# Optimization experiments

Measured on AMD Instinct MI355X. Metric: run time of the kernel, lower is better.

Reference implementation:

```python
import jax, jax.numpy as jnp
import numpy as np

S, R, CM, CZ, C, H = 128, 256, 256, 128, 32, 8
EPS = 1e-5


def layer_norm(x, w, b):
    mu = jnp.mean(x, axis=-1, keepdims=True)
    var = jnp.mean(jnp.square(x - mu), axis=-1, keepdims=True)
    return (x - mu) * jax.lax.rsqrt(var + EPS) * w + b


def setup_inputs() -> dict:
    key = jax.random.key(0)
    ks = jax.random.split(key, 10)
    s = 0.02
    return {
        "m": jax.random.normal(ks[0], (S, R, CM), jnp.float32),
        "z": jax.random.normal(ks[1], (R, R, CZ), jnp.float32),
        "ln_m_w": jnp.ones((CM,), jnp.float32),
        "ln_m_b": jnp.zeros((CM,), jnp.float32),
        "ln_z_w": jnp.ones((CZ,), jnp.float32),
        "ln_z_b": jnp.zeros((CZ,), jnp.float32),
        "Wz": jax.random.normal(ks[2], (CZ, H), jnp.float32) * s,
        "Wq": jax.random.normal(ks[3], (CM, H * C), jnp.float32) * s,
        "Wk": jax.random.normal(ks[4], (CM, H * C), jnp.float32) * s,
        "Wv": jax.random.normal(ks[5], (CM, H * C), jnp.float32) * s,
        "Wg": jax.random.normal(ks[6], (CM, H * C), jnp.float32) * s,
        "bg": jnp.ones((H * C,), jnp.float32),
        "Wo": jax.random.normal(ks[7], (H * C, CM), jnp.float32) * s,
        "bo": jnp.zeros((CM,), jnp.float32),
    }


def reference(m, z, ln_m_w, ln_m_b, ln_z_w, ln_z_b, Wz, Wq, Wk, Wv, Wg, bg, Wo, bo):
    mn = layer_norm(m, ln_m_w, ln_m_b)              # [S,R,CM]
    zn = layer_norm(z, ln_z_w, ln_z_b)              # [R,R,CZ]
    bias = jnp.einsum('qkz,zh->hqk', zn, Wz)        # [H,R,R] pair bias
    q = (mn @ Wq).reshape(S, R, H, C) * (C ** -0.5)
    k = (mn @ Wk).reshape(S, R, H, C)
    v = (mn @ Wv).reshape(S, R, H, C)
    logits = jnp.einsum('sqhc,skhc->shqk', q, k) + bias[None]  # [S,H,R,R]
    a = jax.nn.softmax(logits, axis=-1)
    o = jnp.einsum('shqk,skhc->sqhc', a, v)         # [S,R,H,C]
    g = jax.nn.sigmoid(mn @ Wg + bg).reshape(S, R, H, C)
    return (g * o).reshape(S, R, H * C) @ Wo + bo   # [S,R,CM]
```

## Files before the change

kernel.cpp:

```cpp
#include <hip/hip_runtime.h>
#include <math.h>

#define S_DIM 128
#define R_DIM 256
#define CM_DIM 256
#define CZ_DIM 128
#define C_DIM 32
#define H_DIM 8
#define HC_DIM 256
#define LN_EPS 1e-5f
#define ZPAD 132
#define HSZ 1048576
#define BIAS_SCALE 16384.0f
#define BIAS_INV (1.0f / 16384.0f)

typedef _Float16 half8 __attribute__((ext_vector_type(8)));
typedef _Float16 half4 __attribute__((ext_vector_type(4)));
typedef float f32x4 __attribute__((ext_vector_type(4)));
typedef short short4v __attribute__((ext_vector_type(4)));
typedef short short8v __attribute__((ext_vector_type(8)));

__device__ __forceinline__ float wave_sum(float v) {
#pragma unroll
    for (int off = 32; off > 0; off >>= 1) v += __shfl_down(v, off);
    return v;
}

__global__ __launch_bounds__(256) void convert_w_kernel(const float* __restrict__ Wq,
                                                        const float* __restrict__ Wk,
                                                        const float* __restrict__ Wv,
                                                        const float* __restrict__ Wg,
                                                        const float* __restrict__ Wo,
                                                        _Float16* __restrict__ w3) {
    int kb = blockIdx.x;
    int mat = blockIdx.y;
    const float* src = (mat == 0) ? Wq : (mat == 1) ? Wk : (mat == 2) ? Wv : (mat == 3) ? Wg : Wo;
    int n = threadIdx.x;
    _Float16 tmp[32];
#pragma unroll
    for (int kk = 0; kk < 32; kk++)
        tmp[kk] = (_Float16)src[(size_t)(kb * 32 + kk) * 256 + n];
    half8* dst = (half8*)(w3 + (size_t)mat * 65536 + (size_t)kb * 8192 + (size_t)n * 32);
#pragma unroll
    for (int i = 0; i < 4; i++) dst[i] = *(half8*)&tmp[i * 8];
}

__global__ __launch_bounds__(64) void prep_wz_kernel(const float* __restrict__ w,
                                                     const float* __restrict__ b,
                                                     const float* __restrict__ Wz,
                                                     float* __restrict__ u_g,
                                                     float* __restrict__ UB) {
    int lane = threadIdx.x;
    float w0 = w[lane], w1 = w[lane + 64];
    float b0 = b[lane], b1 = b[lane + 64];
#pragma unroll
    for (int h = 0; h < H_DIM; h++) {
        float wz0 = Wz[lane * H_DIM + h], wz1 = Wz[(lane + 64) * H_DIM + h];
        float u0 = w0 * wz0, u1 = w1 * wz1;
        u_g[h * ZPAD + lane] = u0;
        u_g[h * ZPAD + lane + 64] = u1;
        float U = wave_sum(u0 + u1);
        float B = wave_sum(b0 * wz0 + b1 * wz1);
        if (lane == 0) { UB[h] = U; UB[8 + h] = B; }
    }
}

__global__ __launch_bounds__(64) void ln_m_kernel(const float* __restrict__ m,
                                                  const float* __restrict__ w,
                                                  const float* __restrict__ b,
                                                  _Float16* __restrict__ mn) {
    int row = blockIdx.x;
    int t = threadIdx.x;
    const float4* mrow = (const float4*)(m + (size_t)row * CM_DIM);
    float4 x = mrow[t];
    float s = x.x + x.y + x.z + x.w;
    float ss = x.x * x.x + x.y * x.y + x.z * x.z + x.w * x.w;
    s = wave_sum(s);
    ss = wave_sum(ss);
    s = __shfl(s, 0);
    ss = __shfl(ss, 0);
    float mean = s * (1.0f / CM_DIM);
    float var = ss * (1.0f / CM_DIM) - mean * mean;
    float rsig = rsqrtf(var + LN_EPS);
    float4 wv = ((const float4*)w)[t];
    float4 bv = ((const float4*)b)[t];
    half4 o;
    o[0] = (_Float16)((x.x - mean) * rsig * wv.x + bv.x);
    o[1] = (_Float16)((x.y - mean) * rsig * wv.y + bv.y);
    o[2] = (_Float16)((x.z - mean) * rsig * wv.z + bv.z);
    o[3] = (_Float16)((x.w - mean) * rsig * wv.w + bv.w);
    *(half4*)(mn + (size_t)row * CM_DIM + t * 4) = o;
}

__global__ __launch_bounds__(256) void ln_z_bias_kernel(const float* __restrict__ z,
                                                        const float* __restrict__ u_g,
                                                        const float* __restrict__ UB,
                                                        short* __restrict__ bias_i) {
    __shared__ __align__(16) float zt[64 * ZPAD];
    __shared__ __align__(16) float ut[8 * ZPAD];
    __shared__ float UBs[16];
    int tid = threadIdx.x;
    int row0 = blockIdx.x * 64;
    for (int i = tid; i < 8 * ZPAD; i += 256) ut[i] = u_g[i];
    if (tid < 16) UBs[tid] = UB[tid];
    const float4* zsrc = (const float4*)(z + (size_t)row0 * CZ_DIM);
#pragma unroll
    for (int i = 0; i < 8; i++) {
        int idx = tid + i * 256;
        float4 v = zsrc[idx];
        int r = idx >> 5, c4 = (idx & 31) * 4;
        *(float4*)&zt[r * ZPAD + c4] = v;
    }
    __syncthreads();
    int r = tid >> 2, p = tid & 3;
    const float* zr = &zt[r * ZPAD];
    const float* u0p = &ut[p * ZPAD];
    const float* u1p = &ut[(p + 4) * ZPAD];
    float s = 0.f, ss = 0.f, a0 = 0.f, a1 = 0.f;
#pragma unroll
    for (int c = 0; c < CZ_DIM; c += 4) {
        float4 x = *(const float4*)&zr[c];
        float4 uu0 = *(const float4*)&u0p[c];
        float4 uu1 = *(const float4*)&u1p[c];
        s += x.x + x.y + x.z + x.w;
        ss += x.x * x.x + x.y * x.y + x.z * x.z + x.w * x.w;
        a0 += x.x * uu0.x + x.y * uu0.y + x.z * uu0.z + x.w * uu0.w;
        a1 += x.x * uu1.x + x.y * uu1.y + x.z * uu1.z + x.w * uu1.w;
    }
    float mu = s * (1.0f / CZ_DIM);
    float var = ss * (1.0f / CZ_DIM) - mu * mu;
    float rsig = rsqrtf(var + LN_EPS);
    int row = row0 + r;
    float b0v = rsig * (a0 - mu * UBs[p]) + UBs[8 + p];
    float b1v = rsig * (a1 - mu * UBs[4 + p]) + UBs[12 + p];
    int i0 = (int)rintf(b0v * BIAS_SCALE);
    int i1 = (int)rintf(b1v * BIAS_SCALE);
    i0 = i0 > 32767 ? 32767 : (i0 < -32768 ? -32768 : i0);
    i1 = i1 > 32767 ? 32767 : (i1 < -32768 ? -32768 : i1);
    bias_i[(size_t)p * 65536 + row] = (short)i0;
    bias_i[(size_t)(p + 4) * 65536 + row] = (short)i1;
}

__global__ __launch_bounds__(256, 3) void proj_mfma_kernel(const _Float16* __restrict__ A,
                                                           const _Float16* __restrict__ w3,
                                                           const float* __restrict__ bg,
                                                           _Float16* __restrict__ qh,
                                                           _Float16* __restrict__ kh,
                                                           _Float16* __restrict__ vh,
                                                           _Float16* __restrict__ gh) {
    __shared__ _Float16 As[64][40];
    __shared__ _Float16 Bs[256][40];
    int mat = blockIdx.y;
    int m0 = blockIdx.x * 64;
    const _Float16* W = w3 + (size_t)mat * 65536;
    _Float16* Out = (mat == 0) ? qh : (mat == 1) ? kh : (mat == 2) ? vh : gh;
    int tid = threadIdx.x;
    int lane = tid & 63, wave = tid >> 6;
    int lrow = lane & 15, lk8 = (lane >> 4) * 8;
    f32x4 acc[4][4];
#pragma unroll
    for (int i = 0; i < 4; i++)
#pragma unroll
        for (int j = 0; j < 4; j++) acc[i][j] = (f32x4){0.f, 0.f, 0.f, 0.f};

    for (int kb = 0; kb < 8; kb++) {
        half8 av = *(const half8*)(A + (size_t)(m0 + (tid >> 2)) * 256 + kb * 32 + (tid & 3) * 8);
        half8 bv[4];
#pragma unroll
        for (int i = 0; i < 4; i++)
            bv[i] = *(const half8*)(W + (size_t)kb * 8192 + (size_t)(i * 256 + tid) * 8);
        __syncthreads();
        *(half8*)&As[tid >> 2][(tid & 3) * 8] = av;
#pragma unroll
        for (int i = 0; i < 4; i++) {
            int c = i * 256 + tid;
            *(half8*)&Bs[c >> 2][(c & 3) * 8] = bv[i];
        }
        __syncthreads();
        half8 af[4], bf[4];
#pragma unroll
        for (int mf = 0; mf < 4; mf++) af[mf] = *(half8*)&As[mf * 16 + lrow][lk8];
#pragma unroll
        for (int nf = 0; nf < 4; nf++) bf[nf] = *(half8*)&Bs[wave * 64 + nf * 16 + lrow][lk8];
#pragma unroll
        for (int mf = 0; mf < 4; mf++)
#pragma unroll
            for (int nf = 0; nf < 4; nf++)
                acc[mf][nf] = __builtin_amdgcn_mfma_f32_16x16x32_f16(af[mf], bf[nf], acc[mf][nf], 0, 0, 0);
    }
    const float qscale = 0.17677669529663687f;
#pragma unroll
    for (int mf = 0; mf < 4; mf++)
#pragma unroll
        for (int nf = 0; nf < 4; nf++)
#pragma unroll
            for (int ri = 0; ri < 4; ri++) {
                int row = m0 + mf * 16 + (lane >> 4) * 4 + ri;
                int col = wave * 64 + nf * 16 + lrow;
                float v = acc[mf][nf][ri];
                if (mat == 0) v *= qscale;
                if (mat == 3) {
                    v = 1.0f / (1.0f + __expf(-(v + bg[col])));
                    Out[(size_t)row * 256 + col] = (_Float16)v;
                } else {
                    Out[(size_t)(col >> 5) * HSZ + (size_t)row * 32 + (col & 31)] = (_Float16)v;
                }
            }
}

__global__ __launch_bounds__(512, 1) void attn_mfma_kernel(const _Float16* __restrict__ qh,
                                                           const _Float16* __restrict__ kh,
                                                           const _Float16* __restrict__ vh,
                                                           const short* __restrict__ bias_i,
                                                           _Float16* __restrict__ oh) {
    __shared__ short bias_s[256][264];
    __shared__ _Float16 K_s[64][40];
    __shared__ _Float16 VT_s[32][72];
    int h = blockIdx.x, sg = blockIdx.y;
    int tid = threadIdx.x;
    int lane = tid & 63, wave = tid >> 6;
    int lrow = lane & 15, g = lane >> 4, lk8 = g * 8;
    int qw = wave * 32;

    const short* bsrc = bias_i + (size_t)h * 65536;
#pragma unroll
    for (int i = 0; i < 16; i++) {
        int e = (tid + i * 512) * 8;
        short8v v = *(const short8v*)(bsrc + e);
        *(short8v*)&bias_s[e >> 8][e & 255] = v;
    }

    const _Float16* qbase = qh + (size_t)h * HSZ;
    const _Float16* kbase = kh + (size_t)h * HSZ;
    const _Float16* vbase = vh + (size_t)h * HSZ;
    _Float16* obase = oh + (size_t)h * HSZ;

    bool isK = (wave < 4);
    int key = (tid & 255) >> 2, koff = (tid & 3) * 8;
    int vkey = tid & 63, vc0 = ((tid >> 6) & 3) * 8;

    for (int si = 0; si < 4; si++) {
        int s = sg * 4 + si;
        half8 qfr[2];
#pragma unroll
        for (int qf = 0; qf < 2; qf++)
            qfr[qf] = *(const half8*)(qbase + (size_t)(s * 256 + qw + qf * 16 + lrow) * 32 + lk8);

        f32x4 oaccT[2][2];
        float m_run[2], l_run[2];
#pragma unroll
        for (int qf = 0; qf < 2; qf++) {
            oaccT[qf][0] = (f32x4){0.f, 0.f, 0.f, 0.f};
            oaccT[qf][1] = (f32x4){0.f, 0.f, 0.f, 0.f};
            m_run[qf] = -1e30f;
            l_run[qf] = 0.f;
        }

        half8 stg;
        if (isK) stg = *(const half8*)(kbase + (size_t)(s * 256 + key) * 32 + koff);
        else     stg = *(const half8*)(vbase + (size_t)(s * 256 + vkey) * 32 + vc0);

        for (int kb = 0; kb < 4; kb++) {
            __syncthreads();
            if (isK) {
                *(half8*)&K_s[key][koff] = stg;
            } else {
#pragma unroll
                for (int j = 0; j < 8; j++) VT_s[vc0 + j][vkey] = stg[j];
            }
            if (kb < 3) {
                int nk = (kb + 1) * 64;
                if (isK) stg = *(const half8*)(kbase + (size_t)(s * 256 + nk + key) * 32 + koff);
                else     stg = *(const half8*)(vbase + (size_t)(s * 256 + nk + vkey) * 32 + vc0);
            }
            __syncthreads();

            half8 kfr[4];
#pragma unroll
            for (int kf = 0; kf < 4; kf++) kfr[kf] = *(half8*)&K_s[kf * 16 + lrow][lk8];

#pragma unroll
            for (int qf = 0; qf < 2; qf++) {
                f32x4 sf[4];
#pragma unroll
                for (int kf = 0; kf < 4; kf++) {
                    f32x4 zero = (f32x4){0.f, 0.f, 0.f, 0.f};
                    sf[kf] = __builtin_amdgcn_mfma_f32_16x16x32_f16(kfr[kf], qfr[qf], zero, 0, 0, 0);
                }
                int q = qw + qf * 16 + lrow;
#pragma unroll
                for (int kf = 0; kf < 4; kf++) {
                    short4v bh = *(short4v*)&bias_s[q][kb * 64 + kf * 16 + 4 * g];
#pragma unroll
                    for (int ri = 0; ri < 4; ri++) sf[kf][ri] += (float)bh[ri] * BIAS_INV;
                }
                float tm = -1e30f;
#pragma unroll
                for (int kf = 0; kf < 4; kf++)
#pragma unroll
                    for (int ri = 0; ri < 4; ri++) tm = fmaxf(tm, sf[kf][ri]);
                tm = fmaxf(tm, __shfl_xor(tm, 16));
                tm = fmaxf(tm, __shfl_xor(tm, 32));
                float nm = fmaxf(m_run[qf], tm);
                float sc = __expf(m_run[qf] - nm);
                m_run[qf] = nm;
                oaccT[qf][0] *= sc;
                oaccT[qf][1] *= sc;
                float p[4][4];
                float rs = 0.f;
#pragma unroll
                for (int kf = 0; kf < 4; kf++)
#pragma unroll
                    for (int ri = 0; ri < 4; ri++) {
                        float pv = __expf(sf[kf][ri] - nm);
                        p[kf][ri] = pv;
                        rs += pv;
                    }
                rs += __shfl_xor(rs, 16);
                rs += __shfl_xor(rs, 32);
                l_run[qf] = l_run[qf] * sc + rs;
                unsigned w8[8];
#pragma unroll
                for (int kf = 0; kf < 4; kf++)
#pragma unroll
                    for (int t = 0; t < 2; t++) {
                        union { _Float16 hh[2]; unsigned u; } pk;
                        pk.hh[0] = (_Float16)p[kf][2 * t];
                        pk.hh[1] = (_Float16)p[kf][2 * t + 1];
                        w8[2 * kf + t] = pk.u;
                    }
#pragma unroll
                for (int ks = 0; ks < 2; ks++) {
                    union { unsigned u[4]; half8 h8; } pb;
#pragma unroll
                    for (int u = 0; u < 4; u++) {
                        int srcl = ((g & 1) * 2 + (u >> 1)) * 16 + lrow;
                        unsigned lo_sh = (unsigned)__shfl((int)w8[4 * ks + (u & 1)], srcl);
                        unsigned hi_sh = (unsigned)__shfl((int)w8[4 * ks + (u & 1) + 2], srcl);
                        pb.u[u] = (g >> 1) ? hi_sh : lo_sh;
                    }
#pragma unroll
                    for (int cf = 0; cf < 2; cf++) {
                        half8 va = *(half8*)&VT_s[cf * 16 + lrow][ks * 32 + lk8];
                        oaccT[qf][cf] =
                            __builtin_amdgcn_mfma_f32_16x16x32_f16(va, pb.h8, oaccT[qf][cf], 0, 0, 0);
                    }
                }
            }
        }
#pragma unroll
        for (int qf = 0; qf < 2; qf++) {
            float inv = 1.0f / l_run[qf];
            int q = qw + qf * 16 + lrow;
#pragma unroll
            for (int cf = 0; cf < 2; cf++) {
                half4 o4;
#pragma unroll
                for (int ri = 0; ri < 4; ri++) o4[ri] = (_Float16)(oaccT[qf][cf][ri] * inv);
                *(half4*)(obase + (size_t)(s * 256 + q) * 32 + cf * 16 + 4 * g) = o4;
            }
        }
    }
}

__global__ __launch_bounds__(256, 3) void out_mfma_kernel(const _Float16* __restrict__ gh,
                                                          const _Float16* __restrict__ oh,
                                                          const _Float16* __restrict__ w3o,
                                                          const float* __restrict__ bo,
                                                          float* __restrict__ out) {
    __shared__ _Float16 As[64][40];
    __shared__ _Float16 Bs[256][40];
    int m0 = blockIdx.x * 64;
    int tid = threadIdx.x;
    int lane = tid & 63, wave = tid >> 6;
    int lrow = lane & 15, lk8 = (lane >> 4) * 8;
    f32x4 acc[4][4];
#pragma unroll
    for (int i = 0; i < 4; i++)
#pragma unroll
        for (int j = 0; j < 4; j++) acc[i][j] = (f32x4){0.f, 0.f, 0.f, 0.f};

    for (int kb = 0; kb < 8; kb++) {
        int arow = m0 + (tid >> 2);
        half8 gv = *(const half8*)(gh + (size_t)arow * 256 + kb * 32 + (tid & 3) * 8);
        half8 ov = *(const half8*)(oh + (size_t)kb * HSZ + (size_t)arow * 32 + (tid & 3) * 8);
        half8 av = gv * ov;
        half8 bv[4];
#pragma unroll
        for (int i = 0; i < 4; i++)
            bv[i] = *(const half8*)(w3o + (size_t)kb * 8192 + (size_t)(i * 256 + tid) * 8);
        __syncthreads();
        *(half8*)&As[tid >> 2][(tid & 3) * 8] = av;
#pragma unroll
        for (int i = 0; i < 4; i++) {
            int c = i * 256 + tid;
            *(half8*)&Bs[c >> 2][(c & 3) * 8] = bv[i];
        }
        __syncthreads();
        half8 af[4], bf[4];
#pragma unroll
        for (int mf = 0; mf < 4; mf++) af[mf] = *(half8*)&As[mf * 16 + lrow][lk8];
#pragma unroll
        for (int nf = 0; nf < 4; nf++) bf[nf] = *(half8*)&Bs[wave * 64 + nf * 16 + lrow][lk8];
#pragma unroll
        for (int mf = 0; mf < 4; mf++)
#pragma unroll
            for (int nf = 0; nf < 4; nf++)
                acc[mf][nf] = __builtin_amdgcn_mfma_f32_16x16x32_f16(af[mf], bf[nf], acc[mf][nf], 0, 0, 0);
    }
#pragma unroll
    for (int mf = 0; mf < 4; mf++)
#pragma unroll
        for (int nf = 0; nf < 4; nf++)
#pragma unroll
            for (int ri = 0; ri < 4; ri++) {
                int row = m0 + mf * 16 + (lane >> 4) * 4 + ri;
                int col = wave * 64 + nf * 16 + lrow;
                out[(size_t)row * 256 + col] = acc[mf][nf][ri] + bo[col];
            }
}

extern "C" void kernel_launch(void* const* d_in, const int* in_sizes, int n_in,
                              void* d_out, int out_size, void* d_ws, size_t ws_size,
                              hipStream_t stream) {
    const float* m = (const float*)d_in[0];
    const float* z = (const float*)d_in[1];
    const float* ln_m_w = (const float*)d_in[2];
    const float* ln_m_b = (const float*)d_in[3];
    const float* ln_z_w = (const float*)d_in[4];
    const float* ln_z_b = (const float*)d_in[5];
    const float* Wz = (const float*)d_in[6];
    const float* Wq = (const float*)d_in[7];
    const float* Wk = (const float*)d_in[8];
    const float* Wv = (const float*)d_in[9];
    const float* Wg = (const float*)d_in[10];
    const float* bg = (const float*)d_in[11];
    const float* Wo = (const float*)d_in[12];
    const float* bo = (const float*)d_in[13];
    float* out = (float*)d_out;

    const size_t NE = (size_t)S_DIM * R_DIM * CM_DIM;
    _Float16* hb = (_Float16*)d_ws;
    _Float16* mn_h = hb;
    _Float16* qh = hb + NE;
    _Float16* kh = hb + 2 * NE;
    _Float16* vh = hb + 3 * NE;
    _Float16* gh = hb + 4 * NE;
    _Float16* oh = hb + 5 * NE;
    _Float16* w3 = hb + 6 * NE;
    float* u_g = (float*)(hb + 6 * NE + 5 * 65536);
    float* UB = u_g + 8 * ZPAD;
    short* bias_i = (short*)(UB + 16);

    hipLaunchKernelGGL(convert_w_kernel, dim3(8, 5), dim3(256), 0, stream,
                       Wq, Wk, Wv, Wg, Wo, w3);
    hipLaunchKernelGGL(prep_wz_kernel, dim3(1), dim3(64), 0, stream,
                       ln_z_w, ln_z_b, Wz, u_g, UB);
    hipLaunchKernelGGL(ln_m_kernel, dim3(S_DIM * R_DIM), dim3(64), 0, stream,
                       m, ln_m_w, ln_m_b, mn_h);
    hipLaunchKernelGGL(ln_z_bias_kernel, dim3(1024), dim3(256), 0, stream,
                       z, u_g, UB, bias_i);
    hipLaunchKernelGGL(proj_mfma_kernel, dim3(512, 4), dim3(256), 0, stream,
                       mn_h, w3, bg, qh, kh, vh, gh);
    hipLaunchKernelGGL(attn_mfma_kernel, dim3(H_DIM, 32), dim3(512), 0, stream,
                       qh, kh, vh, bias_i, oh);
    hipLaunchKernelGGL(out_mfma_kernel, dim3(512), dim3(256), 0, stream,
                       gh, oh, w3 + 4 * 65536, bo, out);
}
```

Baseline: 132.6 us.

## Load MFMA fragments directly from global memory, dropping LDS staging in projection GEMMs

The projection and output GEMM kernels no longer stage A and B tiles through shared memory with two barriers per k-step. Each wave now loads its MFMA fragments straight from global memory, and the k-loop is fully unrolled so the loads can be issued early. This removes the LDS round-trip and the block synchronisation. In exchange, all four waves reload the same A fragments, which raises global/L2 traffic, and the launch_bounds occupancy hint is dropped.

```diff
diff --git a/kernel.cpp b/kernel.cpp
--- a/kernel.cpp
+++ b/kernel.cpp
@@ -141,15 +141,13 @@
     bias_i[(size_t)(p + 4) * 65536 + row] = (short)i1;
 }
 
-__global__ __launch_bounds__(256, 3) void proj_mfma_kernel(const _Float16* __restrict__ A,
-                                                           const _Float16* __restrict__ w3,
-                                                           const float* __restrict__ bg,
-                                                           _Float16* __restrict__ qh,
-                                                           _Float16* __restrict__ kh,
-                                                           _Float16* __restrict__ vh,
-                                                           _Float16* __restrict__ gh) {
-    __shared__ _Float16 As[64][40];
-    __shared__ _Float16 Bs[256][40];
+__global__ __launch_bounds__(256) void proj_mfma_kernel(const _Float16* __restrict__ A,
+                                                        const _Float16* __restrict__ w3,
+                                                        const float* __restrict__ bg,
+                                                        _Float16* __restrict__ qh,
+                                                        _Float16* __restrict__ kh,
+                                                        _Float16* __restrict__ vh,
+                                                        _Float16* __restrict__ gh) {
     int mat = blockIdx.y;
     int m0 = blockIdx.x * 64;
     const _Float16* W = w3 + (size_t)mat * 65536;
@@ -163,25 +161,16 @@
 #pragma unroll
         for (int j = 0; j < 4; j++) acc[i][j] = (f32x4){0.f, 0.f, 0.f, 0.f};
 
+#pragma unroll
     for (int kb = 0; kb < 8; kb++) {
-        half8 av = *(const half8*)(A + (size_t)(m0 + (tid >> 2)) * 256 + kb * 32 + (tid & 3) * 8);
-        half8 bv[4];
-#pragma unroll
-        for (int i = 0; i < 4; i++)
-            bv[i] = *(const half8*)(W + (size_t)kb * 8192 + (size_t)(i * 256 + tid) * 8);
-        __syncthreads();
-        *(half8*)&As[tid >> 2][(tid & 3) * 8] = av;
-#pragma unroll
-        for (int i = 0; i < 4; i++) {
-            int c = i * 256 + tid;
-            *(half8*)&Bs[c >> 2][(c & 3) * 8] = bv[i];
-        }
-        __syncthreads();
         half8 af[4], bf[4];
 #pragma unroll
-        for (int mf = 0; mf < 4; mf++) af[mf] = *(half8*)&As[mf * 16 + lrow][lk8];
-#pragma unroll
-        for (int nf = 0; nf < 4; nf++) bf[nf] = *(half8*)&Bs[wave * 64 + nf * 16 + lrow][lk8];
+        for (int mf = 0; mf < 4; mf++)
+            af[mf] = *(const half8*)(A + (size_t)(m0 + mf * 16 + lrow) * 256 + kb * 32 + lk8);
+#pragma unroll
+        for (int nf = 0; nf < 4; nf++)
+            bf[nf] = *(const half8*)(W + (size_t)kb * 8192 +
+                                     (size_t)(wave * 64 + nf * 16 + lrow) * 32 + lk8);
 #pragma unroll
         for (int mf = 0; mf < 4; mf++)
 #pragma unroll
@@ -363,13 +352,11 @@
     }
 }
 
-__global__ __launch_bounds__(256, 3) void out_mfma_kernel(const _Float16* __restrict__ gh,
-                                                          const _Float16* __restrict__ oh,
-                                                          const _Float16* __restrict__ w3o,
-                                                          const float* __restrict__ bo,
-                                                          float* __restrict__ out) {
-    __shared__ _Float16 As[64][40];
-    __shared__ _Float16 Bs[256][40];
+__global__ __launch_bounds__(256) void out_mfma_kernel(const _Float16* __restrict__ gh,
+                                                       const _Float16* __restrict__ oh,
+                                                       const _Float16* __restrict__ w3o,
+                                                       const float* __restrict__ bo,
+                                                       float* __restrict__ out) {
     int m0 = blockIdx.x * 64;
     int tid = threadIdx.x;
     int lane = tid & 63, wave = tid >> 6;
@@ -380,28 +367,20 @@
 #pragma unroll
         for (int j = 0; j < 4; j++) acc[i][j] = (f32x4){0.f, 0.f, 0.f, 0.f};
 
+#pragma unroll
     for (int kb = 0; kb < 8; kb++) {
-        int arow = m0 + (tid >> 2);
-        half8 gv = *(const half8*)(gh + (size_t)arow * 256 + kb * 32 + (tid & 3) * 8);
-        half8 ov = *(const half8*)(oh + (size_t)kb * HSZ + (size_t)arow * 32 + (tid & 3) * 8);
-        half8 av = gv * ov;
-        half8 bv[4];
-#pragma unroll
-        for (int i = 0; i < 4; i++)
-            bv[i] = *(const half8*)(w3o + (size_t)kb * 8192 + (size_t)(i * 256 + tid) * 8);
-        __syncthreads();
-        *(half8*)&As[tid >> 2][(tid & 3) * 8] = av;
-#pragma unroll
-        for (int i = 0; i < 4; i++) {
-            int c = i * 256 + tid;
-            *(half8*)&Bs[c >> 2][(c & 3) * 8] = bv[i];
+        half8 af[4], bf[4];
+#pragma unroll
+        for (int mf = 0; mf < 4; mf++) {
+            int row = m0 + mf * 16 + lrow;
+            half8 gv = *(const half8*)(gh + (size_t)row * 256 + kb * 32 + lk8);
+            half8 ov = *(const half8*)(oh + (size_t)kb * HSZ + (size_t)row * 32 + lk8);
+            af[mf] = gv * ov;
         }
-        __syncthreads();
-        half8 af[4], bf[4];
-#pragma unroll
-        for (int mf = 0; mf < 4; mf++) af[mf] = *(half8*)&As[mf * 16 + lrow][lk8];
-#pragma unroll
-        for (int nf = 0; nf < 4; nf++) bf[nf] = *(half8*)&Bs[wave * 64 + nf * 16 + lrow][lk8];
+#pragma unroll
+        for (int nf = 0; nf < 4; nf++)
+            bf[nf] = *(const half8*)(w3o + (size_t)kb * 8192 +
+                                     (size_t)(wave * 64 + nf * 16 + lrow) * 32 + lk8);
 #pragma unroll
         for (int mf = 0; mf < 4; mf++)
 #pragma unroll
```

Result: slower. 166.0 us (+25.1%).
